# Optimization experiments

Hardware: AMD Instinct MI355X
Metric: run time of the kernel (lower is better)

## Reference

```python
import jax, jax.numpy as jnp
import numpy as np


def setup_inputs() -> dict:
    key = jax.random.key(0)
    k1, k2, k3 = jax.random.split(key, 3)
    B, S, D, E, F = 4, 2048, 1024, 8, 1024
    x = jax.random.normal(k1, (B, S, D), dtype=jnp.float32)
    Wr = jax.random.normal(k2, (E, D), dtype=jnp.float32) * 0.02
    br = jnp.zeros((E,), dtype=jnp.float32)
    We = jax.random.normal(k3, (E, F, D), dtype=jnp.float32) * 0.02
    be = jnp.zeros((E, F), dtype=jnp.float32)
    return {"x": x, "Wr": Wr, "br": br, "We": We, "be": be, "capacity": 1024}


def reference(x, Wr, br, We, be, capacity):
    B, S, D = x.shape
    E = Wr.shape[0]
    N = B * S
    flat = x.reshape(N, D)
    # Router: softmax then argmax (softmax is monotone, kept for faithfulness)
    probs = jax.nn.softmax(flat @ Wr.T + br, axis=-1)          # [N, E]
    ids = jnp.argmax(probs, axis=-1)                            # [N]
    # Capacity: token kept iff its rank (1-based, in flat token order) within
    # its expert is <= capacity (matches the sequential Python loop semantics).
    onehot = jax.nn.one_hot(ids, E, dtype=jnp.int32)            # [N, E]
    rank = jnp.take_along_axis(jnp.cumsum(onehot, axis=0), ids[:, None], axis=1)[:, 0]
    kept = rank <= capacity                                     # [N]
    # Per-expert linear for all tokens, then select the routed expert's output.
    y_all = jnp.einsum('nd,efd->nef', flat, We) + be            # [N, E, F]
    y = jnp.take_along_axis(y_all, ids[:, None, None], axis=1)[:, 0, :]  # [N, F]
    # Dropped tokens pass through unchanged (F == D here by construction).
    out = jnp.where(kept[:, None], y, flat)
    return out.reshape(B, S, D)
```

## Files before the change

### kernel.cpp

```cpp
#include <hip/hip_runtime.h>
#include <hip/hip_bf16.h>


typedef short short8_t __attribute__((ext_vector_type(8)));
typedef float f32x4_t  __attribute__((ext_vector_type(4)));

#define RCAP 1024
#define NCOPY 128

__global__ __launch_bounds__(256) void prep_kernel(
        const float* __restrict__ x,
        const float* __restrict__ Wr,
        const float* __restrict__ br,
        const float* __restrict__ We,
        int* __restrict__ ids,
        int* __restrict__ blockHist,
        __hip_bfloat16* __restrict__ Wt,
        int N, int D, int F, int nRouter) {
    __shared__ int h8[8];
    __shared__ __hip_bfloat16 tile[64][68];
    int tid  = threadIdx.x;

    if ((int)blockIdx.x < nRouter) {
        int lane = tid & 63;
        int wave = tid >> 6;
        int tbase = blockIdx.x * 16 + wave * 4;
        if (tid < 8) h8[tid] = 0;
        __syncthreads();

        const float4* xp[4];
#pragma unroll
        for (int t = 0; t < 4; ++t) {
            int tk = tbase + t; if (tk >= N) tk = N - 1;
            xp[t] = reinterpret_cast<const float4*>(x + (size_t)tk * D);
        }
        float acc[4][8];
#pragma unroll
        for (int t = 0; t < 4; ++t)
#pragma unroll
            for (int e = 0; e < 8; ++e) acc[t][e] = 0.f;
#pragma unroll
        for (int p = 0; p < 4; ++p) {
            float4 xv[4];
#pragma unroll
            for (int t = 0; t < 4; ++t) xv[t] = xp[t][p * 64 + lane];
#pragma unroll
            for (int e = 0; e < 8; ++e) {
                float4 w = reinterpret_cast<const float4*>(Wr + e * D)[p * 64 + lane];
#pragma unroll
                for (int t = 0; t < 4; ++t)
                    acc[t][e] += xv[t].x * w.x + xv[t].y * w.y
                               + xv[t].z * w.z + xv[t].w * w.w;
            }
        }
#pragma unroll
        for (int t = 0; t < 4; ++t)
#pragma unroll
            for (int e = 0; e < 8; ++e) {
                float s = acc[t][e];
                for (int off = 32; off > 0; off >>= 1)
                    s += __shfl_xor(s, off, 64);
                acc[t][e] = s;
            }
        if (lane == 0) {
#pragma unroll
            for (int t = 0; t < 4; ++t) {
                if (tbase + t >= N) break;
                int best = 0;
                float bv = acc[t][0] + br[0];
#pragma unroll
                for (int e = 1; e < 8; ++e) {
                    float lv = acc[t][e] + br[e];
                    if (lv > bv) { bv = lv; best = e; }
                }
                ids[tbase + t] = best;
                atomicAdd(&h8[best], 1);
            }
        }
        __syncthreads();
        if (tid < 8) blockHist[blockIdx.x * 8 + tid] = h8[tid];
    } else {
        int w   = blockIdx.x - nRouter;
        int e   = w >> 8;
        int rem = w & 255;
        int rt  = rem >> 4, kt = rem & 15;
        int r0  = rt * 64, k0 = kt * 64;

        int r = tid >> 2, q0 = tid & 3;
        const float* src = We + ((size_t)e * F + r0 + r) * D + k0;
#pragma unroll
        for (int q = q0; q < 16; q += 4) {
            float4 v = *(const float4*)(src + q * 4);
            tile[r][q * 4 + 0] = __float2bfloat16(v.x);
            tile[r][q * 4 + 1] = __float2bfloat16(v.y);
            tile[r][q * 4 + 2] = __float2bfloat16(v.z);
            tile[r][q * 4 + 3] = __float2bfloat16(v.w);
        }
        __syncthreads();
#pragma unroll
        for (int i = 0; i < 2; ++i) {
            int c  = i * 256 + tid;
            int kq = c >> 6, rr = c & 63;
            union { __hip_bfloat16 h[8]; uint4 u; } uu;
#pragma unroll
            for (int j = 0; j < 8; ++j) uu.h[j] = tile[rr][kq * 8 + j];
            size_t chunk = ((size_t)e * (D / 8) + (k0 >> 3) + kq) * F + r0 + rr;
            *(uint4*)&Wt[chunk * 8] = uu.u;
        }
    }
}

#define MAXPREPB 512
__global__ void rank_scan_kernel(const int* __restrict__ ids,
                                 const int* __restrict__ blockHist,
                                 const int* __restrict__ capacity,
                                 int* __restrict__ gather,
                                 int* __restrict__ kcnt,
                                 int* __restrict__ dropped,
                                 int* __restrict__ hdr,
                                 int N, int nPrepB) {
    __shared__ int histL[MAXPREPB * 8];
    __shared__ int sOff[8], sTot[8], sDropBase[8], sCap;
    __shared__ int waveHist[4][8];
    int tid  = threadIdx.x;
    int lane = tid & 63;
    int wave = tid >> 6;

    {
        int nv = nPrepB * 8 / 4;
        const int4* src = reinterpret_cast<const int4*>(blockHist);
        int4* dst = reinterpret_cast<int4*>(histL);
        for (int i = tid; i < nv; i += 256) dst[i] = src[i];
    }
    __syncthreads();

    if (tid < 8) {
        int bound = blockIdx.x * 16;
        int run = 0, mine = 0;
#pragma unroll 8
        for (int bb = 0; bb < nPrepB; ++bb) {
            if (bb == bound) mine = run;
            run += histL[bb * 8 + tid];
        }
        sOff[tid] = mine;
        sTot[tid] = run;
    }
    __syncthreads();
    if (tid == 0) {
        int cap = capacity[0];
        if (cap > RCAP) cap = RCAP;
        sCap = cap;
        int dbase = 0;
#pragma unroll
        for (int e = 0; e < 8; ++e) {
            sDropBase[e] = dbase;
            int tot = sTot[e];
            if (blockIdx.x == 0) kcnt[e] = tot < cap ? tot : cap;
            dbase += tot > cap ? tot - cap : 0;
        }
        if (blockIdx.x == 0) hdr[0] = dbase;
    }
    __syncthreads();

    int n  = blockIdx.x * 256 + tid;
    int id = (n < N) ? ids[n] : -1;
    int within = 0;
    unsigned long long lt = (1ull << lane) - 1ull;
#pragma unroll
    for (int e = 0; e < 8; ++e) {
        unsigned long long m = __ballot(id == e);
        if (lane == e) waveHist[wave][e] = __popcll(m);
        if (id == e)   within = __popcll(m & lt);
    }
    __syncthreads();
    if (n < N) {
        int prior = sOff[id];
        for (int w = 0; w < wave; ++w) prior += waveHist[w][id];
        int rank = prior + within + 1;
        if (rank <= sCap) {
            gather[id * N + (rank - 1)] = n;
        } else {
            dropped[sDropBase[id] + (rank - sCap - 1)] = n;
        }
    }
}

__global__ __launch_bounds__(256) void packA_kernel(
        const float* __restrict__ x,
        const int* __restrict__ gather,
        const int* __restrict__ kcnt,
        __hip_bfloat16* __restrict__ Xt,
        int N, int D) {
    __shared__ __hip_bfloat16 tile[64][68];
    int w   = blockIdx.x;
    int e   = w >> 8;
    int rem = w & 255;
    int rt  = rem >> 4, kt = rem & 15;
    int r0  = rt * 64, k0 = kt * 64;
    int tid = threadIdx.x;
    int cnt = kcnt[e];
    if (r0 >= cnt) return;

    int r = tid >> 2, q0 = tid & 3;
    int gr = r0 + r;
    if (gr < cnt) {
        const float* src = x + (size_t)gather[e * N + gr] * D + k0;
#pragma unroll
        for (int q = q0; q < 16; q += 4) {
            float4 v = *(const float4*)(src + q * 4);
            tile[r][q * 4 + 0] = __float2bfloat16(v.x);
            tile[r][q * 4 + 1] = __float2bfloat16(v.y);
            tile[r][q * 4 + 2] = __float2bfloat16(v.z);
            tile[r][q * 4 + 3] = __float2bfloat16(v.w);
        }
    }
    __syncthreads();
#pragma unroll
    for (int i = 0; i < 2; ++i) {
        int c  = i * 256 + tid;
        int kq = c >> 6, rr = c & 63;
        if (r0 + rr >= cnt) continue;
        union { __hip_bfloat16 h[8]; uint4 u; } uu;
#pragma unroll
        for (int j = 0; j < 8; ++j) uu.h[j] = tile[rr][kq * 8 + j];
        size_t chunk = ((size_t)e * (D / 8) + (k0 >> 3) + kq) * RCAP + r0 + rr;
        *(uint4*)&Xt[chunk * 8] = uu.u;
    }
}

#define TM 128
#define TN 128

__global__ __launch_bounds__(256) void expert_gemm_mfma(
        const float* __restrict__ x,
        const __hip_bfloat16* __restrict__ Xt,
        const __hip_bfloat16* __restrict__ Wt,
        const float* __restrict__ be,
        const int* __restrict__ kcnt,
        const int* __restrict__ gather,
        const int* __restrict__ dropped,
        const int* __restrict__ hdr,
        float* __restrict__ out,
        int N, int D, int F, int nGemm) {
    int b = blockIdx.x;
    if (b >= nGemm) {
        int nd = hdr[0];
        for (int i = b - nGemm; i < nd; i += NCOPY) {
            int tok = dropped[i];
            const float4* src = reinterpret_cast<const float4*>(x + (size_t)tok * D);
            float4* dst = reinterpret_cast<float4*>(out + (size_t)tok * D);
            dst[threadIdx.x] = src[threadIdx.x];
        }
        return;
    }

    int e  = b & 7;
    int xt = (b >> 3) & 7;
    int yt = b >> 6;
    int cnt = kcnt[e];
    int row0 = yt * TM;
    if (row0 >= cnt) return;
    int col0 = xt * TN;

    int lane = threadIdx.x & 63;
    int wave = threadIdx.x >> 6;
    int wr = wave >> 1, wc = wave & 1;
    int kq = lane >> 4, fr = lane & 15;

    const short8_t* Ab = (const short8_t*)Xt + (size_t)e * (D / 8) * RCAP;
    const short8_t* Bb = (const short8_t*)Wt + (size_t)e * (D / 8) * F;
    int rowA = row0 + wr * 64 + fr;
    int colB = col0 + wc * 64 + fr;

    f32x4_t zero = {0.f, 0.f, 0.f, 0.f};
    f32x4_t acc[4][4];
#pragma unroll
    for (int m = 0; m < 4; ++m)
#pragma unroll
        for (int n = 0; n < 4; ++n) acc[m][n] = zero;

#define LDFRAG(AV, BV, T) {                                                  \
    _Pragma("unroll")                                                        \
    for (int m = 0; m < 4; ++m)                                              \
        AV[m] = Ab[(size_t)(((T) * 4 + kq) * RCAP) + rowA + m * 16];         \
    _Pragma("unroll")                                                        \
    for (int n = 0; n < 4; ++n)                                              \
        BV[n] = Bb[(size_t)(((T) * 4 + kq) * F) + colB + n * 16]; }

#define DOMFMA(AV, BV) {                                                     \
    _Pragma("unroll")                                                        \
    for (int m = 0; m < 4; ++m)                                              \
        _Pragma("unroll")                                                    \
        for (int n = 0; n < 4; ++n)                                          \
            acc[m][n] = __builtin_amdgcn_mfma_f32_16x16x32_bf16(             \
                AV[m], BV[n], acc[m][n], 0, 0, 0); }

    const int nt = D / 32;
    short8_t a0[4], b0[4], a1[4], b1[4];
    LDFRAG(a0, b0, 0)
    for (int t = 0; t < nt; t += 2) {
        LDFRAG(a1, b1, t + 1)
        DOMFMA(a0, b0)
        if (t + 2 < nt) LDFRAG(a0, b0, t + 2)
        DOMFMA(a1, b1)
    }

    int fcol = colB;
    float bias[4];
#pragma unroll
    for (int n = 0; n < 4; ++n) bias[n] = be[e * F + fcol + n * 16];
#pragma unroll
    for (int m = 0; m < 4; ++m) {
        int gr0 = row0 + wr * 64 + m * 16 + kq * 4;
#pragma unroll
        for (int r = 0; r < 4; ++r) {
            int gr = gr0 + r;
            if (gr >= cnt) continue;
            int tok = gather[e * N + gr];
#pragma unroll
            for (int n = 0; n < 4; ++n)
                out[(size_t)tok * F + fcol + n * 16] = acc[m][n][r] + bias[n];
        }
    }
}

extern "C" void kernel_launch(void* const* d_in, const int* in_sizes, int n_in,
                              void* d_out, int out_size, void* d_ws, size_t ws_size,
                              hipStream_t stream) {
    const float* x        = (const float*)d_in[0];
    const float* Wr       = (const float*)d_in[1];
    const float* br       = (const float*)d_in[2];
    const float* We       = (const float*)d_in[3];
    const float* be       = (const float*)d_in[4];
    const int*   capacity = (const int*)d_in[5];

    int E = in_sizes[2];
    int D = in_sizes[1] / E;
    int N = in_sizes[0] / D;
    int F = in_sizes[4] / E;

    float* out = (float*)d_out;

    int nRouter = (N + 15) / 16;

    char* w = (char*)d_ws;
    size_t off = 0;
    auto take = [&](size_t bytes) {
        size_t p = off;
        off = (off + bytes + 255) & ~(size_t)255;
        return p;
    };
    int* ids       = (int*)(w + take((size_t)N * 4));
    int* blockHist = (int*)(w + take((size_t)nRouter * 8 * 4));
    int* kcnt      = (int*)(w + take(8 * 4));
    int* hdr       = (int*)(w + take(8 * 4));
    int* gather    = (int*)(w + take((size_t)E * N * 4));
    int* dropped   = (int*)(w + take((size_t)N * 4));
    __hip_bfloat16* Xt = (__hip_bfloat16*)(w + take((size_t)E * (D / 8) * RCAP * 8 * 2));
    __hip_bfloat16* Wt = (__hip_bfloat16*)(w + take((size_t)E * (D / 8) * F * 8 * 2));
    (void)off;

    {
        int nWt = E * (F / 64) * (D / 64);
        prep_kernel<<<nRouter + nWt, 256, 0, stream>>>(
            x, Wr, br, We, ids, blockHist, Wt, N, D, F, nRouter);
    }
    rank_scan_kernel<<<(N + 255) / 256, 256, 0, stream>>>(
        ids, blockHist, capacity, gather, kcnt, dropped, hdr, N, nRouter);
    packA_kernel<<<E * (RCAP / 64) * (D / 64), 256, 0, stream>>>(
        x, gather, kcnt, Xt, N, D);
    {
        int nGemm = E * (F / TN) * (RCAP / TM);
        expert_gemm_mfma<<<nGemm + NCOPY, 256, 0, stream>>>(
            x, Xt, Wt, be, kcnt, gather, dropped, hdr, out, N, D, F, nGemm);
    }
}
```

Before: 65.74 us.

## Stage expert GEMM tiles through LDS with async global_load_lds triple buffering

Replaces direct global-to-register fragment loads in the expert GEMM with asynchronous global_load_lds copies into a three-stage LDS ring buffer, synchronised by explicit vmcnt waits and barriers. Each A/B element is fetched once per block into shared memory and reused across waves instead of each wave loading its own fragments, which reduces redundant global/L2 traffic and lets loads overlap MFMA work. It adds LDS usage and a barrier every K step, and relies on hand-written waitcnt counts being correct.

```diff
diff --git a/kernel.cpp b/kernel.cpp
--- a/kernel.cpp
+++ b/kernel.cpp
@@ -7,6 +7,13 @@
 
 #define RCAP 1024
 #define NCOPY 128
+
+typedef const unsigned int __attribute__((address_space(1))) gu32;
+typedef unsigned int       __attribute__((address_space(3))) lu32;
+
+__device__ __forceinline__ void async_load16(const void* gptr, void* lptr) {
+    __builtin_amdgcn_global_load_lds((gu32*)gptr, (lu32*)lptr, 16, 0, 0);
+}
 
 __global__ __launch_bounds__(256) void prep_kernel(
         const float* __restrict__ x,
@@ -230,6 +237,7 @@
 
 #define TM 128
 #define TN 128
+#define TK 32
 
 __global__ __launch_bounds__(256) void expert_gemm_mfma(
         const float* __restrict__ x,
@@ -262,15 +270,41 @@
     if (row0 >= cnt) return;
     int col0 = xt * TN;
 
-    int lane = threadIdx.x & 63;
-    int wave = threadIdx.x >> 6;
+    __shared__ __hip_bfloat16 As[3][4][TM][8];
+    __shared__ __hip_bfloat16 Bs[3][4][TN][8];
+
+    int tid  = threadIdx.x;
+    int lane = tid & 63;
+    int wave = tid >> 6;
     int wr = wave >> 1, wc = wave & 1;
     int kq = lane >> 4, fr = lane & 15;
-
-    const short8_t* Ab = (const short8_t*)Xt + (size_t)e * (D / 8) * RCAP;
-    const short8_t* Bb = (const short8_t*)Wt + (size_t)e * (D / 8) * F;
-    int rowA = row0 + wr * 64 + fr;
-    int colB = col0 + wc * 64 + fr;
+    int rA = wr * 64 + fr;
+    int rB = wc * 64 + fr;
+
+    const __hip_bfloat16* pa[2];
+    const __hip_bfloat16* pb[2];
+#pragma unroll
+    for (int rd = 0; rd < 2; ++rd) {
+        int c = rd * 256 + tid;
+        int kqr = c >> 7, rr = c & 127;
+        pa[rd] = Xt + (((size_t)e * (D / 8) + kqr) * RCAP + row0 + rr) * 8;
+        pb[rd] = Wt + (((size_t)e * (D / 8) + kqr) * F    + col0 + rr) * 8;
+    }
+    const size_t strA = (size_t)4 * RCAP * 8;
+    const size_t strB = (size_t)4 * F * 8;
+
+    auto stage = [&](int buf, int t) {
+#pragma unroll
+        for (int rd = 0; rd < 2; ++rd) {
+            char* la = (char*)&As[buf][0][0][0] + (size_t)(rd * 256 + wave * 64) * 16;
+            async_load16(pa[rd] + (size_t)t * strA, la);
+        }
+#pragma unroll
+        for (int rd = 0; rd < 2; ++rd) {
+            char* lb = (char*)&Bs[buf][0][0][0] + (size_t)(rd * 256 + wave * 64) * 16;
+            async_load16(pb[rd] + (size_t)t * strB, lb);
+        }
+    };
 
     f32x4_t zero = {0.f, 0.f, 0.f, 0.f};
     f32x4_t acc[4][4];
@@ -279,33 +313,35 @@
 #pragma unroll
         for (int n = 0; n < 4; ++n) acc[m][n] = zero;
 
-#define LDFRAG(AV, BV, T) {                                                  \
-    _Pragma("unroll")                                                        \
-    for (int m = 0; m < 4; ++m)                                              \
-        AV[m] = Ab[(size_t)(((T) * 4 + kq) * RCAP) + rowA + m * 16];         \
-    _Pragma("unroll")                                                        \
-    for (int n = 0; n < 4; ++n)                                              \
-        BV[n] = Bb[(size_t)(((T) * 4 + kq) * F) + colB + n * 16]; }
-
-#define DOMFMA(AV, BV) {                                                     \
-    _Pragma("unroll")                                                        \
-    for (int m = 0; m < 4; ++m)                                              \
-        _Pragma("unroll")                                                    \
-        for (int n = 0; n < 4; ++n)                                          \
-            acc[m][n] = __builtin_amdgcn_mfma_f32_16x16x32_bf16(             \
-                AV[m], BV[n], acc[m][n], 0, 0, 0); }
-
-    const int nt = D / 32;
-    short8_t a0[4], b0[4], a1[4], b1[4];
-    LDFRAG(a0, b0, 0)
-    for (int t = 0; t < nt; t += 2) {
-        LDFRAG(a1, b1, t + 1)
-        DOMFMA(a0, b0)
-        if (t + 2 < nt) LDFRAG(a0, b0, t + 2)
-        DOMFMA(a1, b1)
-    }
-
-    int fcol = colB;
+    const int nt = D / TK;
+    stage(0, 0);
+    stage(1, 1);
+
+    for (int t = 0; t < nt; ++t) {
+        if (t + 1 < nt) {
+            asm volatile("s_waitcnt vmcnt(4)\n\ts_barrier" ::: "memory");
+        } else {
+            asm volatile("s_waitcnt vmcnt(0)\n\ts_barrier" ::: "memory");
+        }
+        if (t + 2 < nt) stage((t + 2) % 3, t + 2);
+
+        int cb = t % 3;
+        short8_t af[4], bf[4];
+#pragma unroll
+        for (int m = 0; m < 4; ++m)
+            af[m] = *(const short8_t*)&As[cb][kq][rA + m * 16][0];
+#pragma unroll
+        for (int n = 0; n < 4; ++n)
+            bf[n] = *(const short8_t*)&Bs[cb][kq][rB + n * 16][0];
+#pragma unroll
+        for (int m = 0; m < 4; ++m)
+#pragma unroll
+            for (int n = 0; n < 4; ++n)
+                acc[m][n] = __builtin_amdgcn_mfma_f32_16x16x32_bf16(
+                    af[m], bf[n], acc[m][n], 0, 0, 0);
+    }
+
+    int fcol = col0 + wc * 64 + fr;
     float bias[4];
 #pragma unroll
     for (int n = 0; n < 4; ++n) bias[n] = be[e * F + fcol + n * 16];
```

Measured after the change: 69.24 us. 1.05x slower.
